# Kernel tuning notes

Measured on AMD Instinct MI355X. Metric: run time of the kernel, lower is better.

## Reference

```python
import jax, jax.numpy as jnp
import numpy as np

H = 64          # hiddens_dims
K = 3           # Chebyshev order
B = 16          # graphs in batch
NPG = 16384     # nodes per graph
N = B * NPG     # total nodes
E = 2_097_152   # total edges
R = 2191        # num_residues (hard-coded in source)
E_REF = R * 16
HALF = N // 2   # backbone count == sidechain count (mask is balanced per graph)


def _lin(k, fan_in, shape):
    return jax.random.uniform(k, shape, jnp.float32, -1.0, 1.0) / np.sqrt(fan_in)


def setup_inputs() -> dict:
    key = jax.random.key(0)
    ks = jax.random.split(key, 40)
    inp = {}
    inp["x"] = jax.random.normal(ks[0], (N, 3), jnp.float32)
    inp["edge_index"] = jax.random.randint(ks[1], (2, E), 0, N)
    inp["batch"] = jnp.repeat(jnp.arange(B, dtype=jnp.int32), NPG)
    blk = jnp.concatenate([jnp.ones((NPG // 2,), bool), jnp.zeros((NPG // 2,), bool)])
    inp["mask"] = jnp.tile(blk, B)  # backbone=True first half of each graph block
    inp["x_ref"] = jax.random.normal(ks[2], (R, 3), jnp.float32)
    inp["edgeref"] = jax.random.randint(ks[3], (2, E_REF), 0, R)
    i = 4
    for name, cin in [("cw0", 3), ("cw1", H), ("cw2", H), ("rw0", 3), ("rw1", H), ("rw2", H)]:
        inp[name] = _lin(ks[i], cin, (K, cin, H)); i += 1
        inp[name.replace("w", "b")] = jnp.zeros((H,), jnp.float32)  # ChebConv bias init = zeros
    for name, cin, cout in [("mlp_w", 2 * H, H), ("mlpP2_w", 2 * H, H),
                            ("rep0_w", H, H), ("rep1_w", H, H), ("rep2_w", H, 3)]:
        inp[name] = _lin(ks[i], cin, (cin, cout)); i += 1
        inp[name.replace("_w", "_b")] = _lin(ks[i], cin, (cout,)); i += 1
    return inp


def cheb_conv(x, edge_index, W, b, n):
    # PyG ChebConv with sym normalization, lambda_max=2: L_hat = -D^-1/2 A D^-1/2 (diag = 0)
    row, col = edge_index[0], edge_index[1]
    deg = jax.ops.segment_sum(jnp.ones_like(x[:, 0])[row] * 0 + 1.0, row, num_segments=n)
    dinv = jnp.where(deg > 0, jax.lax.rsqrt(jnp.maximum(deg, 1e-12)), 0.0)
    w = -(dinv[row] * dinv[col])  # [E]

    def prop(h):  # L_hat @ h via gather + segment_sum
        return jax.ops.segment_sum(w[:, None] * h[col], row, num_segments=n)

    Tx0 = x
    out = Tx0 @ W[0]
    Tx1 = prop(x)
    out = out + Tx1 @ W[1]
    for k in range(2, K):
        Tx2 = 2.0 * prop(Tx1) - Tx0
        out = out + Tx2 @ W[k]
        Tx0, Tx1 = Tx1, Tx2
    return out + b


def _forward(x, edge_index, mask, x_ref, edgeref,
             cw0, cb0, cw1, cb1, cw2, cb2, rw0, rb0, rw1, rb1, rw2, rb2,
             mlp_w, mlp_b, mlpP2_w, mlpP2_b,
             rep0_w, rep0_b, rep1_w, rep1_b, rep2_w, rep2_b):
    # main GNN stack (tanh after all but last; dropout is identity in eval)
    h = jnp.tanh(cheb_conv(x, edge_index, cw0, cb0, N))
    h = jnp.tanh(cheb_conv(h, edge_index, cw1, cb1, N))
    h = cheb_conv(h, edge_index, cw2, cb2, N)

    bb_idx = jnp.nonzero(mask, size=HALF)[0]
    sc_idx = jnp.nonzero(~mask, size=HALF)[0]
    x_bb = h[bb_idx].reshape(B, -1, H).mean(axis=1)[:, None, :]  # [B,1,H]
    x_sc = h[sc_idx].reshape(B, -1, H).mean(axis=1)[:, None, :]  # [B,1,H]

    # reference-graph stack: source bug makes `conv2 != self.convs[-1]` always True,
    # so tanh follows every convRef layer
    r = jnp.tanh(cheb_conv(x_ref, edgeref, rw0, rb0, R))
    r = jnp.tanh(cheb_conv(r, edgeref, rw1, rb1, R))
    r = jnp.tanh(cheb_conv(r, edgeref, rw2, rb2, R))
    r = jnp.broadcast_to(r[None], (B, R, H))

    bb_rep = jnp.broadcast_to(x_bb, (B, R, H))
    phase1 = jnp.concatenate([r, bb_rep], axis=-1) @ mlp_w + mlp_b        # [B,R,H]
    sc_rep = jnp.broadcast_to(x_sc, (B, R, H))
    phase2 = jnp.concatenate([phase1, sc_rep], axis=-1) @ mlpP2_w + mlpP2_b  # [B,R,H]

    res = phase2.reshape(-1, H)
    res = jax.nn.relu(res @ rep0_w + rep0_b)
    res = jax.nn.relu(res @ rep1_w + rep1_b)
    res = jax.nn.relu(res @ rep2_w + rep2_b)  # [B*R, 3]
    return res.reshape(-1, 3), x_bb, x_sc


def reference(x, edge_index, batch, mask, x_ref, edgeref,
              cw0, cb0, cw1, cb1, cw2, cb2, rw0, rb0, rw1, rb1, rw2, rb2,
              mlp_w, mlp_b, mlpP2_w, mlpP2_b,
              rep0_w, rep0_b, rep1_w, rep1_b, rep2_w, rep2_b):
    del batch  # only used for len(batch.unique()) == B, a static constant here
    return _forward(x, edge_index, mask, x_ref, edgeref,
                    cw0, cb0, cw1, cb1, cw2, cb2, rw0, rb0, rw1, rb1, rw2, rb2,
                    mlp_w, mlp_b, mlpP2_w, mlpP2_b,
                    rep0_w, rep0_b, rep1_w, rep1_b, rep2_w, rep2_b)
```

## Files before the change

kernel.cpp:

```cpp
#include <hip/hip_runtime.h>
#include <hip/hip_fp16.h>
#include <math.h>

#define NN 262144
#define NE 2097152
#define RR 2191
#define ER (RR*16)
#define NB 16
#define BRR (NB*RR)
#define OUT_RES (BRR*3)

typedef __attribute__((ext_vector_type(8))) _Float16 half8;
typedef __attribute__((ext_vector_type(4))) float f32x4;

__global__ void k_hist(const int* __restrict__ row, int* __restrict__ deg, int nE){
  int i = blockIdx.x*blockDim.x + threadIdx.x;
  int st = gridDim.x*blockDim.x;
  for (; i < nE; i += st) atomicAdd(&deg[row[i]], 1);
}

__global__ void k_dinv(const int* __restrict__ deg, float* __restrict__ dinv, int n){
  int i = blockIdx.x*blockDim.x + threadIdx.x;
  if (i < n){ int d = deg[i]; dinv[i] = d > 0 ? 1.0f/sqrtf((float)d) : 0.0f; }
}

__global__ void k_scan1(const int* __restrict__ deg, int* __restrict__ rowptr, int* __restrict__ partials){
  __shared__ int s[256];
  int t = threadIdx.x; int i = blockIdx.x*256 + t;
  int v = deg[i]; s[t] = v; __syncthreads();
  for (int off = 1; off < 256; off <<= 1){
    int x = (t >= off) ? s[t-off] : 0; __syncthreads();
    s[t] += x; __syncthreads();
  }
  rowptr[i] = s[t] - v;
  if (t == 255) partials[blockIdx.x] = s[255];
}

__global__ void k_scan2(int* __restrict__ partials){
  __shared__ int s[1024];
  int t = threadIdx.x; int v = partials[t]; s[t] = v; __syncthreads();
  for (int off = 1; off < 1024; off <<= 1){
    int x = (t >= off) ? s[t-off] : 0; __syncthreads();
    s[t] += x; __syncthreads();
  }
  partials[t] = s[t] - v;
}

__global__ void k_scan3(int* __restrict__ rowptr, const int* __restrict__ partials){
  int t = threadIdx.x; int i = blockIdx.x*256 + t;
  rowptr[i] += partials[blockIdx.x];
  if (i == 0) rowptr[NN] = NE;
}

__global__ void k_scan_small(const int* __restrict__ deg, int* __restrict__ rowptr, int n){
  __shared__ int s[256];
  int t = threadIdx.x;
  int carry = 0;
  for (int base = 0; base < n; base += 256){
    int idx = base + t;
    int v = (idx < n) ? deg[idx] : 0;
    s[t] = v; __syncthreads();
    for (int off = 1; off < 256; off <<= 1){
      int x = (t >= off) ? s[t-off] : 0; __syncthreads();
      s[t] += x; __syncthreads();
    }
    if (idx < n) rowptr[idx] = carry + s[t] - v;
    carry += s[255];
    __syncthreads();
  }
  if (t == 0) rowptr[n] = carry;
}

__global__ void k_scatter(const int* __restrict__ row, const int* __restrict__ col,
                          const float* __restrict__ dinv, const int* __restrict__ rowptr,
                          int* __restrict__ cursor, int2* __restrict__ pair, int nE){
  int i = blockIdx.x*blockDim.x + threadIdx.x;
  int st = gridDim.x*blockDim.x;
  for (; i < nE; i += st){
    int r = row[i], c = col[i];
    int pos = rowptr[r] + atomicAdd(&cursor[r], 1);
    pair[pos] = make_int2(c, __float_as_int(-dinv[r]*dinv[c]));
  }
}

__global__ void k_prop3(const float* __restrict__ h, float* __restrict__ y,
                        const int* __restrict__ rowptr, const int2* __restrict__ pair, int n){
  int i = blockIdx.x*blockDim.x + threadIdx.x;
  if (i >= n) return;
  float a0 = 0.f, a1 = 0.f, a2 = 0.f;
  int s = rowptr[i], e = rowptr[i+1];
  int p = s;
  for (; p + 4 <= e; p += 4){
    int2 q0 = pair[p], q1 = pair[p+1], q2 = pair[p+2], q3 = pair[p+3];
    float w0 = __int_as_float(q0.y), w1 = __int_as_float(q1.y);
    float w2 = __int_as_float(q2.y), w3 = __int_as_float(q3.y);
    float x00=h[q0.x*3+0], x01=h[q0.x*3+1], x02=h[q0.x*3+2];
    float x10=h[q1.x*3+0], x11=h[q1.x*3+1], x12=h[q1.x*3+2];
    float x20=h[q2.x*3+0], x21=h[q2.x*3+1], x22=h[q2.x*3+2];
    float x30=h[q3.x*3+0], x31=h[q3.x*3+1], x32=h[q3.x*3+2];
    a0 = fmaf(w0,x00, fmaf(w1,x10, fmaf(w2,x20, fmaf(w3,x30, a0))));
    a1 = fmaf(w0,x01, fmaf(w1,x11, fmaf(w2,x21, fmaf(w3,x31, a1))));
    a2 = fmaf(w0,x02, fmaf(w1,x12, fmaf(w2,x22, fmaf(w3,x32, a2))));
  }
  for (; p < e; p++){
    int2 q = pair[p]; float wv = __int_as_float(q.y);
    a0 = fmaf(wv, h[q.x*3+0], a0); a1 = fmaf(wv, h[q.x*3+1], a1); a2 = fmaf(wv, h[q.x*3+2], a2);
  }
  y[i*3+0] = a0; y[i*3+1] = a1; y[i*3+2] = a2;
}

__global__ void k_prop64(const float* __restrict__ h, float* __restrict__ y,
                         const int* __restrict__ rowptr, const int2* __restrict__ pair, int n){
  int t = threadIdx.x, lane = t & 63;
  int i = blockIdx.x*4 + (t >> 6);
  if (i >= n) return;
  float acc = 0.f;
  int s = rowptr[i], e = rowptr[i+1];
  int p = s;
  for (; p + 4 <= e; p += 4){
    int2 q0 = pair[p], q1 = pair[p+1], q2 = pair[p+2], q3 = pair[p+3];
    float v0 = h[(size_t)q0.x*64 + lane], v1 = h[(size_t)q1.x*64 + lane];
    float v2 = h[(size_t)q2.x*64 + lane], v3 = h[(size_t)q3.x*64 + lane];
    acc = fmaf(__int_as_float(q0.y),v0, fmaf(__int_as_float(q1.y),v1,
          fmaf(__int_as_float(q2.y),v2, fmaf(__int_as_float(q3.y),v3, acc))));
  }
  for (; p < e; p++){
    int2 q = pair[p];
    acc = fmaf(__int_as_float(q.y), h[(size_t)q.x*64 + lane], acc);
  }
  y[(size_t)i*64 + lane] = acc;
}

__global__ void __launch_bounds__(256) k_prop64h(
    const uint2* __restrict__ h2, uint2* __restrict__ y2,
    const int* __restrict__ rowptr, const int2* __restrict__ pair, int n){
  int t = threadIdx.x;
  int sub = t & 15;
  int row = blockIdx.x*16 + (t >> 4);
  if (row >= n) return;
  int s = rowptr[row], e = rowptr[row+1];
  float a0=0.f, a1=0.f, a2=0.f, a3=0.f;
  int p = s;
  for (; p + 4 <= e; p += 4){
    int2 q0 = pair[p], q1 = pair[p+1], q2 = pair[p+2], q3 = pair[p+3];
    uint2 v0 = h2[(size_t)q0.x*16 + sub];
    uint2 v1 = h2[(size_t)q1.x*16 + sub];
    uint2 v2 = h2[(size_t)q2.x*16 + sub];
    uint2 v3 = h2[(size_t)q3.x*16 + sub];
    float w0 = __int_as_float(q0.y), w1 = __int_as_float(q1.y);
    float w2 = __int_as_float(q2.y), w3 = __int_as_float(q3.y);
    float2 f0a = __half22float2(*(__half2*)&v0.x), f0b = __half22float2(*(__half2*)&v0.y);
    float2 f1a = __half22float2(*(__half2*)&v1.x), f1b = __half22float2(*(__half2*)&v1.y);
    float2 f2a = __half22float2(*(__half2*)&v2.x), f2b = __half22float2(*(__half2*)&v2.y);
    float2 f3a = __half22float2(*(__half2*)&v3.x), f3b = __half22float2(*(__half2*)&v3.y);
    a0 = fmaf(w0,f0a.x, fmaf(w1,f1a.x, fmaf(w2,f2a.x, fmaf(w3,f3a.x, a0))));
    a1 = fmaf(w0,f0a.y, fmaf(w1,f1a.y, fmaf(w2,f2a.y, fmaf(w3,f3a.y, a1))));
    a2 = fmaf(w0,f0b.x, fmaf(w1,f1b.x, fmaf(w2,f2b.x, fmaf(w3,f3b.x, a2))));
    a3 = fmaf(w0,f0b.y, fmaf(w1,f1b.y, fmaf(w2,f2b.y, fmaf(w3,f3b.y, a3))));
  }
  for (; p < e; p++){
    int2 q = pair[p];
    float wv = __int_as_float(q.y);
    uint2 v = h2[(size_t)q.x*16 + sub];
    float2 fa = __half22float2(*(__half2*)&v.x), fb = __half22float2(*(__half2*)&v.y);
    a0 = fmaf(wv, fa.x, a0); a1 = fmaf(wv, fa.y, a1);
    a2 = fmaf(wv, fb.x, a2); a3 = fmaf(wv, fb.y, a3);
  }
  __half2 lo = __floats2half2_rn(a0, a1), hi = __floats2half2_rn(a2, a3);
  uint2 r; r.x = *(unsigned*)&lo; r.y = *(unsigned*)&hi;
  y2[(size_t)row*16 + sub] = r;
}

__global__ void k_combine3f(const float* __restrict__ x, const float* __restrict__ t1,
                            const float* __restrict__ t2, const float* __restrict__ W,
                            const float* __restrict__ bias, float* __restrict__ out, int n){
  int t = threadIdx.x, lane = t & 63;
  int i = blockIdx.x*4 + (t >> 6);
  if (i >= n) return;
  float acc = bias[lane];
  #pragma unroll
  for (int j = 0; j < 3; j++){
    float x0 = x[i*3+j], x1 = t1[i*3+j];
    float x2 = 2.0f*t2[i*3+j] - x0;
    acc += x0*W[      j*64 + lane]
         + x1*W[192 + j*64 + lane]
         + x2*W[384 + j*64 + lane];
  }
  out[(size_t)i*64 + lane] = tanhf(acc);
}

__global__ void k_combine3h(const float* __restrict__ x, const float* __restrict__ t1,
                            const float* __restrict__ t2, const float* __restrict__ W,
                            const float* __restrict__ bias, __half* __restrict__ out, int n){
  int t = threadIdx.x, lane = t & 63;
  int i = blockIdx.x*4 + (t >> 6);
  if (i >= n) return;
  float acc = bias[lane];
  #pragma unroll
  for (int j = 0; j < 3; j++){
    float x0 = x[i*3+j], x1 = t1[i*3+j];
    float x2 = 2.0f*t2[i*3+j] - x0;
    acc += x0*W[      j*64 + lane]
         + x1*W[192 + j*64 + lane]
         + x2*W[384 + j*64 + lane];
  }
  out[(size_t)i*64 + lane] = __float2half_rn(tanhf(acc));
}

__global__ void k_weff(const float* __restrict__ W, float* __restrict__ D){
  int i = blockIdx.x*blockDim.x + threadIdx.x;
  D[i]        = W[i] - W[8192 + i];
  D[4096 + i] = W[4096 + i];
  D[8192 + i] = 2.0f * W[8192 + i];
}

__global__ void k_wpack(const float* __restrict__ W, _Float16* __restrict__ D){
  int t = blockIdx.x*blockDim.x + threadIdx.x;
  int reg = t & 7, lane = (t >> 3) & 63, nt = (t >> 9) & 3, kc = t >> 11;
  int m = kc >> 1;
  int kin = (kc & 1)*32 + ((lane >> 4) & 3)*8 + reg;
  int n = nt*16 + (lane & 15);
  float eff;
  if      (m == 0) eff = W[kin*64 + n] - W[8192 + kin*64 + n];
  else if (m == 1) eff = W[4096 + kin*64 + n];
  else             eff = 2.0f * W[8192 + kin*64 + n];
  D[t] = (_Float16)eff;
}

__global__ void __launch_bounds__(256) k_combine64m(
    const __half* A, const __half* B, const __half* C,
    const _Float16* __restrict__ wfrag, const float* __restrict__ bias,
    __half* out, int ntiles, int wavestride){
  int t = threadIdx.x;
  int lane = t & 63;
  int wv = blockIdx.x*4 + (t >> 6);
  half8 bf[24];
  #pragma unroll
  for (int i = 0; i < 24; i++)
    bf[i] = *(const half8*)(wfrag + ((size_t)(i*64 + lane))*8);
  int col = lane & 15, grp = (lane >> 4) & 3;
  float b0 = bias[col], b1 = bias[16+col], b2 = bias[32+col], b3 = bias[48+col];
  for (int tile = wv; tile < ntiles; tile += wavestride){
    size_t rb = (size_t)tile*16;
    f32x4 acc0 = {b0,b0,b0,b0}, acc1 = {b1,b1,b1,b1};
    f32x4 acc2 = {b2,b2,b2,b2}, acc3 = {b3,b3,b3,b3};
    #pragma unroll
    for (int kc = 0; kc < 6; kc++){
      const __half* s = (kc < 2) ? A : (kc < 4) ? B : C;
      half8 a = *(const half8*)(s + (rb + col)*64 + (kc & 1)*32 + grp*8);
      acc0 = __builtin_amdgcn_mfma_f32_16x16x32_f16(a, bf[kc*4+0], acc0, 0,0,0);
      acc1 = __builtin_amdgcn_mfma_f32_16x16x32_f16(a, bf[kc*4+1], acc1, 0,0,0);
      acc2 = __builtin_amdgcn_mfma_f32_16x16x32_f16(a, bf[kc*4+2], acc2, 0,0,0);
      acc3 = __builtin_amdgcn_mfma_f32_16x16x32_f16(a, bf[kc*4+3], acc3, 0,0,0);
    }
    __half* o = out + (rb + grp*4)*64;
    #pragma unroll
    for (int r = 0; r < 4; r++){
      o[(size_t)r*64 +      col] = __float2half_rn(tanhf(acc0[r]));
      o[(size_t)r*64 + 16 + col] = __float2half_rn(tanhf(acc1[r]));
      o[(size_t)r*64 + 32 + col] = __float2half_rn(tanhf(acc2[r]));
      o[(size_t)r*64 + 48 + col] = __float2half_rn(tanhf(acc3[r]));
    }
  }
}

__global__ void k_pool3(const __half2* __restrict__ hA, const __half2* __restrict__ hB,
                        const __half2* __restrict__ hC, float* __restrict__ pA,
                        float* __restrict__ pB, float* __restrict__ pC){
  const __half2* src = (blockIdx.y == 0) ? hA : (blockIdx.y == 1) ? hB : hC;
  float* dst         = (blockIdx.y == 0) ? pA : (blockIdx.y == 1) ? pB : pC;
  int blk = blockIdx.x;
  int chunk = blk & 15, seg = blk >> 4;
  int t = threadIdx.x, ch2 = t & 31, rsub = t >> 5;
  int base = seg*8192 + chunk*512;
  float ax = 0.f, ay = 0.f;
  for (int j = 0; j < 64; j++){
    int row = base + rsub + j*8;
    float2 v = __half22float2(src[(size_t)row*32 + ch2]);
    ax += v.x; ay += v.y;
  }
  __shared__ float sx[256], sy[256];
  sx[t] = ax; sy[t] = ay; __syncthreads();
  if (t < 32){
    float tx = 0.f, ty = 0.f;
    #pragma unroll
    for (int j = 0; j < 8; j++){ tx += sx[ch2 + j*32]; ty += sy[ch2 + j*32]; }
    int b = seg >> 1, half_ = seg & 1;
    atomicAdd(&dst[half_*1024 + b*64 + ch2*2],     tx);
    atomicAdd(&dst[half_*1024 + b*64 + ch2*2 + 1], ty);
  }
}

__global__ void k_combine_pooled(const float* __restrict__ pA, const float* __restrict__ pB,
                                 const float* __restrict__ pC, const float* __restrict__ weff,
                                 const float* __restrict__ bias, float* __restrict__ xbbsc,
                                 float* __restrict__ dout){
  int i = blockIdx.x*blockDim.x + threadIdx.x;
  int pr = i >> 6, c = i & 63;
  const float* a = pA + pr*64;
  const float* b = pB + pr*64;
  const float* cc = pC + pr*64;
  float v = 0.f;
  for (int k = 0; k < 64; k++){
    v = fmaf(a[k],  weff[        k*64 + c], v);
    v = fmaf(b[k],  weff[4096 +  k*64 + c], v);
    v = fmaf(cc[k], weff[8192 +  k*64 + c], v);
  }
  v = v*(1.0f/8192.0f) + bias[c];
  xbbsc[i] = v;
  dout[OUT_RES + i] = v;
}

__global__ void __launch_bounds__(256) k_combine64f(
    const float* __restrict__ A, const float* __restrict__ Bm, const float* __restrict__ C,
    const float* __restrict__ Weff, const float* __restrict__ bias,
    float* __restrict__ out, int n){
  int t = threadIdx.x;
  int lane = t & 63;
  int wid  = __builtin_amdgcn_readfirstlane(t >> 6);
  int half_ = wid & 1;
  int row  = blockIdx.x*128 + (wid >> 1)*64 + lane;
  bool active = (row < n);
  float acc[32];
  #pragma unroll
  for (int c = 0; c < 32; c++) acc[c] = bias[half_*32 + c];
  if (active){
    #pragma unroll 1
    for (int m = 0; m < 3; m++){
      const float* src = (m == 0 ? A : (m == 1 ? Bm : C)) + (size_t)row*64;
      const float* Wm  = Weff + m*4096 + half_*32;
      #pragma unroll 1
      for (int k4 = 0; k4 < 16; k4++){
        float4 a4 = *(const float4*)(src + k4*4);
        const float* wk = Wm + k4*256;
        #pragma unroll
        for (int kk = 0; kk < 4; kk++){
          float a = (kk == 0) ? a4.x : (kk == 1) ? a4.y : (kk == 2) ? a4.z : a4.w;
          #pragma unroll
          for (int c = 0; c < 32; c++)
            acc[c] = fmaf(a, wk[kk*64 + c], acc[c]);
        }
      }
    }
  }
  __syncthreads();
  if (active){
    float* o = out + (size_t)row*64 + half_*32;
    #pragma unroll
    for (int c = 0; c < 32; c++) o[c] = tanhf(acc[c]);
  }
}

__global__ void k_matrows(const float* __restrict__ in, const float* __restrict__ W,
                          const float* __restrict__ bias, float* __restrict__ out,
                          int n, int accum){
  int t = threadIdx.x, lane = t & 63;
  int i = blockIdx.x*4 + (t >> 6);
  if (i >= n) return;
  float v = in[i*64 + lane];
  float acc = bias ? bias[lane] : 0.0f;
  #pragma unroll
  for (int k = 0; k < 64; k++) acc += __shfl(v, k, 64) * W[k*64 + lane];
  if (accum) acc += out[i*64 + lane];
  out[i*64 + lane] = acc;
}

__global__ void k_final(const float* __restrict__ rt3, const float* __restrict__ bt3,
                        const float* __restrict__ W1, const float* __restrict__ b1,
                        const float* __restrict__ W2, const float* __restrict__ b2,
                        float* __restrict__ dout){
  int t = threadIdx.x, lane = t & 63;
  int g = blockIdx.x*4 + (t >> 6);
  if (g >= BRR) return;
  int b = g / RR, r = g - b*RR;
  float m = rt3[r*64 + lane] + bt3[b*64 + lane];
  m = fmaxf(m, 0.0f);
  float acc = b1[lane];
  #pragma unroll
  for (int k = 0; k < 64; k++) acc += __shfl(m, k, 64) * W1[k*64 + lane];
  float u = fmaxf(acc, 0.0f);
  float p0 = u*W2[lane*3+0], p1 = u*W2[lane*3+1], p2 = u*W2[lane*3+2];
  #pragma unroll
  for (int off = 32; off > 0; off >>= 1){
    p0 += __shfl_xor(p0, off, 64);
    p1 += __shfl_xor(p1, off, 64);
    p2 += __shfl_xor(p2, off, 64);
  }
  if (lane == 0){
    dout[g*3+0] = fmaxf(p0 + b2[0], 0.0f);
    dout[g*3+1] = fmaxf(p1 + b2[1], 0.0f);
    dout[g*3+2] = fmaxf(p2 + b2[2], 0.0f);
  }
}

extern "C" void kernel_launch(void* const* d_in, const int* in_sizes, int n_in,
                              void* d_out, int out_size, void* d_ws, size_t ws_size,
                              hipStream_t stream){
  const float* x     = (const float*)d_in[0];
  const int*   eidx  = (const int*)d_in[1];
  const float* x_ref = (const float*)d_in[4];
  const int*   eref  = (const int*)d_in[5];
  const float* cw0 = (const float*)d_in[6],  *cb0 = (const float*)d_in[7];
  const float* cw1 = (const float*)d_in[8],  *cb1 = (const float*)d_in[9];
  const float* cw2 = (const float*)d_in[10], *cb2 = (const float*)d_in[11];
  const float* rw0 = (const float*)d_in[12], *rb0 = (const float*)d_in[13];
  const float* rw1 = (const float*)d_in[14], *rb1 = (const float*)d_in[15];
  const float* rw2 = (const float*)d_in[16], *rb2 = (const float*)d_in[17];
  const float* mlp_w  = (const float*)d_in[18], *mlp_b  = (const float*)d_in[19];
  const float* mlp2_w = (const float*)d_in[20], *mlp2_b = (const float*)d_in[21];
  const float* rep0_w = (const float*)d_in[22], *rep0_b = (const float*)d_in[23];
  const float* rep1_w = (const float*)d_in[24], *rep1_b = (const float*)d_in[25];
  const float* rep2_w = (const float*)d_in[26], *rep2_b = (const float*)d_in[27];
  float* out = (float*)d_out;

  char* w = (char*)d_ws;
  size_t off = 0;
  auto alloc = [&](size_t bytes)->void*{
    void* p = w + off;
    off = (off + bytes + 255) & ~(size_t)255;
    return p;
  };
  int*   deg     = (int*)  alloc(NN*4);
  int*   cursor  = (int*)  alloc(NN*4);
  int*   degR    = (int*)  alloc(RR*4);
  int*   cursorR = (int*)  alloc(RR*4);
  float* poolA   = (float*)alloc(2048*4);
  float* poolB   = (float*)alloc(2048*4);
  float* poolC   = (float*)alloc(2048*4);
  size_t zero_bytes = off;

  int*   rowptr   = (int*)  alloc((NN+1)*4);
  int*   partials = (int*)  alloc(1024*4);
  int*   rowptrR  = (int*)  alloc((RR+1)*4);
  float* dinv     = (float*)alloc(NN*4);
  float* dinvR    = (float*)alloc(RR*4);
  int2*  cpair    = (int2*) alloc((size_t)NE*8);
  int2*  cpairR   = (int2*) alloc((size_t)ER*8);
  float* t1_3     = (float*)alloc((size_t)NN*3*4);
  float* t2_3     = (float*)alloc((size_t)NN*3*4);
  float* rt1_3    = (float*)alloc(RR*3*4);
  float* rt2_3    = (float*)alloc(RR*3*4);
  __half* hA      = (__half*)alloc((size_t)NN*64*2);
  __half* hB      = (__half*)alloc((size_t)NN*64*2);
  __half* hC      = (__half*)alloc((size_t)NN*64*2);
  float* refA     = (float*)alloc(RR*64*4);
  float* refB     = (float*)alloc(RR*64*4);
  float* refC     = (float*)alloc(RR*64*4);
  float* xbbsc    = (float*)alloc(2048*4);
  float* rterm    = (float*)alloc(RR*64*4);
  float* bbterm   = (float*)alloc(NB*64*4);
  float* rt2a     = (float*)alloc(RR*64*4);
  float* bt2a     = (float*)alloc(NB*64*4);
  float* rt3a     = (float*)alloc(RR*64*4);
  float* bt3a     = (float*)alloc(NB*64*4);
  float* weffC2   = (float*)alloc(12288*4);
  float* weffR1   = (float*)alloc(12288*4);
  float* weffR2   = (float*)alloc(12288*4);
  _Float16* wfragC1 = (_Float16*)alloc(12288*2);
  (void)ws_size; (void)in_sizes; (void)n_in; (void)out_size;

  hipMemsetAsync(d_ws, 0, zero_bytes, stream);

  k_weff<<<16, 256, 0, stream>>>(cw2, weffC2);
  k_weff<<<16, 256, 0, stream>>>(rw1, weffR1);
  k_weff<<<16, 256, 0, stream>>>(rw2, weffR2);
  k_wpack<<<48, 256, 0, stream>>>(cw1, wfragC1);

  k_hist<<<2048, 256, 0, stream>>>(eidx, deg, NE);
  k_hist<<<64,   256, 0, stream>>>(eref, degR, ER);
  k_dinv<<<1024, 256, 0, stream>>>(deg, dinv, NN);
  k_dinv<<<9,    256, 0, stream>>>(degR, dinvR, RR);
  k_scan1<<<1024, 256, 0, stream>>>(deg, rowptr, partials);
  k_scan2<<<1, 1024, 0, stream>>>(partials);
  k_scan3<<<1024, 256, 0, stream>>>(rowptr, partials);
  k_scan_small<<<1, 256, 0, stream>>>(degR, rowptrR, RR);
  k_scatter<<<2048, 256, 0, stream>>>(eidx, eidx+NE, dinv, rowptr, cursor, cpair, NE);
  k_scatter<<<64,   256, 0, stream>>>(eref, eref+ER, dinvR, rowptrR, cursorR, cpairR, ER);

  k_prop3<<<1024, 256, 0, stream>>>(x, t1_3, rowptr, cpair, NN);
  k_prop3<<<1024, 256, 0, stream>>>(t1_3, t2_3, rowptr, cpair, NN);
  k_combine3h<<<NN/4, 256, 0, stream>>>(x, t1_3, t2_3, cw0, cb0, hA, NN);
  k_prop64h<<<NN/16, 256, 0, stream>>>((const uint2*)hA, (uint2*)hB, rowptr, cpair, NN);
  k_prop64h<<<NN/16, 256, 0, stream>>>((const uint2*)hB, (uint2*)hC, rowptr, cpair, NN);
  k_combine64m<<<1024, 256, 0, stream>>>(hA, hB, hC, wfragC1, cb1, hA, NN/16, 4096);
  k_prop64h<<<NN/16, 256, 0, stream>>>((const uint2*)hA, (uint2*)hB, rowptr, cpair, NN);
  k_prop64h<<<NN/16, 256, 0, stream>>>((const uint2*)hB, (uint2*)hC, rowptr, cpair, NN);
  k_pool3<<<dim3(512,3), 256, 0, stream>>>((const __half2*)hA, (const __half2*)hB,
                                           (const __half2*)hC, poolA, poolB, poolC);
  k_combine_pooled<<<8, 256, 0, stream>>>(poolA, poolB, poolC, weffC2, cb2, xbbsc, out);

  k_prop3<<<9, 256, 0, stream>>>(x_ref, rt1_3, rowptrR, cpairR, RR);
  k_prop3<<<9, 256, 0, stream>>>(rt1_3, rt2_3, rowptrR, cpairR, RR);
  k_combine3f<<<548, 256, 0, stream>>>(x_ref, rt1_3, rt2_3, rw0, rb0, refA, RR);
  k_prop64<<<548, 256, 0, stream>>>(refA, refB, rowptrR, cpairR, RR);
  k_prop64<<<548, 256, 0, stream>>>(refB, refC, rowptrR, cpairR, RR);
  k_combine64f<<<(RR+127)/128, 256, 0, stream>>>(refA, refB, refC, weffR1, rb1, refA, RR);
  k_prop64<<<548, 256, 0, stream>>>(refA, refB, rowptrR, cpairR, RR);
  k_prop64<<<548, 256, 0, stream>>>(refB, refC, rowptrR, cpairR, RR);
  k_combine64f<<<(RR+127)/128, 256, 0, stream>>>(refA, refB, refC, weffR2, rb2, refA, RR);

  k_matrows<<<548, 256, 0, stream>>>(refA,   mlp_w,        nullptr, rterm,  RR, 0);
  k_matrows<<<4,   256, 0, stream>>>(xbbsc,  mlp_w+4096,   mlp_b,   bbterm, NB, 0);
  k_matrows<<<548, 256, 0, stream>>>(rterm,  mlp2_w,       nullptr, rt2a,   RR, 0);
  k_matrows<<<4,   256, 0, stream>>>(bbterm, mlp2_w,       nullptr, bt2a,   NB, 0);
  k_matrows<<<4,   256, 0, stream>>>(xbbsc+1024, mlp2_w+4096, mlp2_b, bt2a, NB, 1);
  k_matrows<<<548, 256, 0, stream>>>(rt2a,   rep0_w,       nullptr, rt3a,   RR, 0);
  k_matrows<<<4,   256, 0, stream>>>(bt2a,   rep0_w,       rep0_b,  bt3a,   NB, 0);

  k_final<<<(BRR+3)/4, 256, 0, stream>>>(rt3a, bt3a, rep1_w, rep1_b, rep2_w, rep2_b, out);
}
```

Baseline: 760.1 us.

## Two-pass bucketed CSR build, fuse dinv into scans, fuse MLP chains, wider gather unroll

Replaces the per-row atomic scatter for the CSR build with a two-pass scheme. Edges are first binned into 64-row buckets through a small atomic counter array, then a per-bucket kernel places them into rows using shared-memory cursors. This is meant to cut contention on global atomics and scattered writes, at the cost of an extra staging buffer and an extra pass over the edges. The dinv computation is folded into the scan kernels, the seven small matrix-row launches become two chained kernels, and the fp16 propagation gather is unrolled to 8 edges for more memory-level parallelism.

```diff
diff --git a/kernel.cpp b/kernel.cpp
--- a/kernel.cpp
+++ b/kernel.cpp
@@ -9,6 +9,7 @@
 #define NB 16
 #define BRR (NB*RR)
 #define OUT_RES (BRR*3)
+#define NBKT 4096
 
 typedef __attribute__((ext_vector_type(8))) _Float16 half8;
 typedef __attribute__((ext_vector_type(4))) float f32x4;
@@ -19,15 +20,12 @@
   for (; i < nE; i += st) atomicAdd(&deg[row[i]], 1);
 }
 
-__global__ void k_dinv(const int* __restrict__ deg, float* __restrict__ dinv, int n){
-  int i = blockIdx.x*blockDim.x + threadIdx.x;
-  if (i < n){ int d = deg[i]; dinv[i] = d > 0 ? 1.0f/sqrtf((float)d) : 0.0f; }
-}
-
-__global__ void k_scan1(const int* __restrict__ deg, int* __restrict__ rowptr, int* __restrict__ partials){
+__global__ void k_scan1(const int* __restrict__ deg, int* __restrict__ rowptr,
+                        int* __restrict__ partials, float* __restrict__ dinv){
   __shared__ int s[256];
   int t = threadIdx.x; int i = blockIdx.x*256 + t;
   int v = deg[i]; s[t] = v; __syncthreads();
+  dinv[i] = v > 0 ? 1.0f/sqrtf((float)v) : 0.0f;
   for (int off = 1; off < 256; off <<= 1){
     int x = (t >= off) ? s[t-off] : 0; __syncthreads();
     s[t] += x; __syncthreads();
@@ -52,13 +50,15 @@
   if (i == 0) rowptr[NN] = NE;
 }
 
-__global__ void k_scan_small(const int* __restrict__ deg, int* __restrict__ rowptr, int n){
+__global__ void k_scan_small(const int* __restrict__ deg, int* __restrict__ rowptr,
+                             float* __restrict__ dinv, int n){
   __shared__ int s[256];
   int t = threadIdx.x;
   int carry = 0;
   for (int base = 0; base < n; base += 256){
     int idx = base + t;
     int v = (idx < n) ? deg[idx] : 0;
+    if (idx < n) dinv[idx] = v > 0 ? 1.0f/sqrtf((float)v) : 0.0f;
     s[t] = v; __syncthreads();
     for (int off = 1; off < 256; off <<= 1){
       int x = (t >= off) ? s[t-off] : 0; __syncthreads();
@@ -71,9 +71,44 @@
   if (t == 0) rowptr[n] = carry;
 }
 
-__global__ void k_scatter(const int* __restrict__ row, const int* __restrict__ col,
-                          const float* __restrict__ dinv, const int* __restrict__ rowptr,
-                          int* __restrict__ cursor, int2* __restrict__ pair, int nE){
+__global__ void k_binA(const int* __restrict__ row, const int* __restrict__ col,
+                       const float* __restrict__ dinv, const int* __restrict__ rowptr,
+                       int* __restrict__ bcur, int2* __restrict__ staging, int nE){
+  int i = blockIdx.x*blockDim.x + threadIdx.x;
+  int st = gridDim.x*blockDim.x;
+  for (; i < nE; i += st){
+    int r = row[i], c = col[i];
+    int b = r >> 6;
+    int pos = rowptr[b << 6] + atomicAdd(&bcur[b], 1);
+    float wv = -dinv[r]*dinv[c];
+    staging[pos] = make_int2(((r & 63) << 24) | c, __float_as_int(wv));
+  }
+}
+
+__global__ void __launch_bounds__(256) k_binB(const int2* __restrict__ staging,
+                                              const int* __restrict__ rowptr,
+                                              int2* __restrict__ cpair){
+  __shared__ int rp[65];
+  __shared__ int rowcur[64];
+  int b = blockIdx.x;
+  int t = threadIdx.x;
+  if (t < 64){ rowcur[t] = 0; rp[t] = rowptr[(b << 6) + t]; }
+  if (t == 64) rp[64] = rowptr[(b << 6) + 64];
+  __syncthreads();
+  int base = rp[0];
+  int n_b = rp[64] - base;
+  for (int i = t; i < n_b; i += 256){
+    int2 pr = staging[base + i];
+    int rl = (pr.x >> 24) & 63;
+    int c  = pr.x & 0xFFFFFF;
+    int idx = atomicAdd(&rowcur[rl], 1);
+    cpair[rp[rl] + idx] = make_int2(c, pr.y);
+  }
+}
+
+__global__ void k_scatter_ref(const int* __restrict__ row, const int* __restrict__ col,
+                              const float* __restrict__ dinv, const int* __restrict__ rowptr,
+                              int* __restrict__ cursor, int2* __restrict__ pair, int nE){
   int i = blockIdx.x*blockDim.x + threadIdx.x;
   int st = gridDim.x*blockDim.x;
   for (; i < nE; i += st){
@@ -141,22 +176,35 @@
   int s = rowptr[row], e = rowptr[row+1];
   float a0=0.f, a1=0.f, a2=0.f, a3=0.f;
   int p = s;
+  for (; p + 8 <= e; p += 8){
+    int2 q[8]; uint2 v[8];
+    #pragma unroll
+    for (int j = 0; j < 8; j++) q[j] = pair[p+j];
+    #pragma unroll
+    for (int j = 0; j < 8; j++) v[j] = h2[(size_t)q[j].x*16 + sub];
+    #pragma unroll
+    for (int j = 0; j < 8; j++){
+      float wv = __int_as_float(q[j].y);
+      float2 fa = __half22float2(*(__half2*)&v[j].x);
+      float2 fb = __half22float2(*(__half2*)&v[j].y);
+      a0 = fmaf(wv, fa.x, a0); a1 = fmaf(wv, fa.y, a1);
+      a2 = fmaf(wv, fb.x, a2); a3 = fmaf(wv, fb.y, a3);
+    }
+  }
   for (; p + 4 <= e; p += 4){
-    int2 q0 = pair[p], q1 = pair[p+1], q2 = pair[p+2], q3 = pair[p+3];
-    uint2 v0 = h2[(size_t)q0.x*16 + sub];
-    uint2 v1 = h2[(size_t)q1.x*16 + sub];
-    uint2 v2 = h2[(size_t)q2.x*16 + sub];
-    uint2 v3 = h2[(size_t)q3.x*16 + sub];
-    float w0 = __int_as_float(q0.y), w1 = __int_as_float(q1.y);
-    float w2 = __int_as_float(q2.y), w3 = __int_as_float(q3.y);
-    float2 f0a = __half22float2(*(__half2*)&v0.x), f0b = __half22float2(*(__half2*)&v0.y);
-    float2 f1a = __half22float2(*(__half2*)&v1.x), f1b = __half22float2(*(__half2*)&v1.y);
-    float2 f2a = __half22float2(*(__half2*)&v2.x), f2b = __half22float2(*(__half2*)&v2.y);
-    float2 f3a = __half22float2(*(__half2*)&v3.x), f3b = __half22float2(*(__half2*)&v3.y);
-    a0 = fmaf(w0,f0a.x, fmaf(w1,f1a.x, fmaf(w2,f2a.x, fmaf(w3,f3a.x, a0))));
-    a1 = fmaf(w0,f0a.y, fmaf(w1,f1a.y, fmaf(w2,f2a.y, fmaf(w3,f3a.y, a1))));
-    a2 = fmaf(w0,f0b.x, fmaf(w1,f1b.x, fmaf(w2,f2b.x, fmaf(w3,f3b.x, a2))));
-    a3 = fmaf(w0,f0b.y, fmaf(w1,f1b.y, fmaf(w2,f2b.y, fmaf(w3,f3b.y, a3))));
+    int2 q[4]; uint2 v[4];
+    #pragma unroll
+    for (int j = 0; j < 4; j++) q[j] = pair[p+j];
+    #pragma unroll
+    for (int j = 0; j < 4; j++) v[j] = h2[(size_t)q[j].x*16 + sub];
+    #pragma unroll
+    for (int j = 0; j < 4; j++){
+      float wv = __int_as_float(q[j].y);
+      float2 fa = __half22float2(*(__half2*)&v[j].x);
+      float2 fb = __half22float2(*(__half2*)&v[j].y);
+      a0 = fmaf(wv, fa.x, a0); a1 = fmaf(wv, fa.y, a1);
+      a2 = fmaf(wv, fb.x, a2); a3 = fmaf(wv, fb.y, a3);
+    }
   }
   for (; p < e; p++){
     int2 q = pair[p];
@@ -351,18 +399,47 @@
   }
 }
 
-__global__ void k_matrows(const float* __restrict__ in, const float* __restrict__ W,
-                          const float* __restrict__ bias, float* __restrict__ out,
-                          int n, int accum){
+__global__ void k_refchain(const float* __restrict__ refA, const float* __restrict__ mlp_w,
+                           const float* __restrict__ mlp2_w, const float* __restrict__ rep0_w,
+                           float* __restrict__ rt3a, int n){
   int t = threadIdx.x, lane = t & 63;
   int i = blockIdx.x*4 + (t >> 6);
   if (i >= n) return;
-  float v = in[i*64 + lane];
-  float acc = bias ? bias[lane] : 0.0f;
-  #pragma unroll
-  for (int k = 0; k < 64; k++) acc += __shfl(v, k, 64) * W[k*64 + lane];
-  if (accum) acc += out[i*64 + lane];
-  out[i*64 + lane] = acc;
+  float v = refA[i*64 + lane];
+  float a = 0.f;
+  #pragma unroll
+  for (int k = 0; k < 64; k++) a += __shfl(v, k, 64) * mlp_w[k*64 + lane];
+  float b = 0.f;
+  #pragma unroll
+  for (int k = 0; k < 64; k++) b += __shfl(a, k, 64) * mlp2_w[k*64 + lane];
+  float c = 0.f;
+  #pragma unroll
+  for (int k = 0; k < 64; k++) c += __shfl(b, k, 64) * rep0_w[k*64 + lane];
+  rt3a[i*64 + lane] = c;
+}
+
+__global__ void k_bbchain(const float* __restrict__ xbbsc,
+                          const float* __restrict__ mlp_w,  const float* __restrict__ mlp_b,
+                          const float* __restrict__ mlp2_w, const float* __restrict__ mlp2_b,
+                          const float* __restrict__ rep0_w, const float* __restrict__ rep0_b,
+                          float* __restrict__ bt3a){
+  int t = threadIdx.x, lane = t & 63;
+  int i = blockIdx.x*4 + (t >> 6);
+  if (i >= NB) return;
+  float vbb = xbbsc[i*64 + lane];
+  float vsc = xbbsc[1024 + i*64 + lane];
+  float a = mlp_b[lane];
+  #pragma unroll
+  for (int k = 0; k < 64; k++) a += __shfl(vbb, k, 64) * mlp_w[4096 + k*64 + lane];
+  float b = mlp2_b[lane];
+  #pragma unroll
+  for (int k = 0; k < 64; k++) b += __shfl(a, k, 64) * mlp2_w[k*64 + lane];
+  #pragma unroll
+  for (int k = 0; k < 64; k++) b += __shfl(vsc, k, 64) * mlp2_w[4096 + k*64 + lane];
+  float c = rep0_b[lane];
+  #pragma unroll
+  for (int k = 0; k < 64; k++) c += __shfl(b, k, 64) * rep0_w[k*64 + lane];
+  bt3a[i*64 + lane] = c;
 }
 
 __global__ void k_final(const float* __restrict__ rt3, const float* __restrict__ bt3,
@@ -421,7 +498,7 @@
     return p;
   };
   int*   deg     = (int*)  alloc(NN*4);
-  int*   cursor  = (int*)  alloc(NN*4);
+  int*   bcur    = (int*)  alloc(NBKT*4);
   int*   degR    = (int*)  alloc(RR*4);
   int*   cursorR = (int*)  alloc(RR*4);
   float* poolA   = (float*)alloc(2048*4);
@@ -434,6 +511,7 @@
   int*   rowptrR  = (int*)  alloc((RR+1)*4);
   float* dinv     = (float*)alloc(NN*4);
   float* dinvR    = (float*)alloc(RR*4);
+  int2*  staging  = (int2*) alloc((size_t)NE*8);
   int2*  cpair    = (int2*) alloc((size_t)NE*8);
   int2*  cpairR   = (int2*) alloc((size_t)ER*8);
   float* t1_3     = (float*)alloc((size_t)NN*3*4);
@@ -447,10 +525,6 @@
   float* refB     = (float*)alloc(RR*64*4);
   float* refC     = (float*)alloc(RR*64*4);
   float* xbbsc    = (float*)alloc(2048*4);
-  float* rterm    = (float*)alloc(RR*64*4);
-  float* bbterm   = (float*)alloc(NB*64*4);
-  float* rt2a     = (float*)alloc(RR*64*4);
-  float* bt2a     = (float*)alloc(NB*64*4);
   float* rt3a     = (float*)alloc(RR*64*4);
   float* bt3a     = (float*)alloc(NB*64*4);
   float* weffC2   = (float*)alloc(12288*4);
@@ -468,14 +542,13 @@
 
   k_hist<<<2048, 256, 0, stream>>>(eidx, deg, NE);
   k_hist<<<64,   256, 0, stream>>>(eref, degR, ER);
-  k_dinv<<<1024, 256, 0, stream>>>(deg, dinv, NN);
-  k_dinv<<<9,    256, 0, stream>>>(degR, dinvR, RR);
-  k_scan1<<<1024, 256, 0, stream>>>(deg, rowptr, partials);
+  k_scan1<<<1024, 256, 0, stream>>>(deg, rowptr, partials, dinv);
   k_scan2<<<1, 1024, 0, stream>>>(partials);
   k_scan3<<<1024, 256, 0, stream>>>(rowptr, partials);
-  k_scan_small<<<1, 256, 0, stream>>>(degR, rowptrR, RR);
-  k_scatter<<<2048, 256, 0, stream>>>(eidx, eidx+NE, dinv, rowptr, cursor, cpair, NE);
-  k_scatter<<<64,   256, 0, stream>>>(eref, eref+ER, dinvR, rowptrR, cursorR, cpairR, ER);
+  k_scan_small<<<1, 256, 0, stream>>>(degR, rowptrR, dinvR, RR);
+  k_binA<<<2048, 256, 0, stream>>>(eidx, eidx+NE, dinv, rowptr, bcur, staging, NE);
+  k_binB<<<NBKT, 256, 0, stream>>>(staging, rowptr, cpair);
+  k_scatter_ref<<<64, 256, 0, stream>>>(eref, eref+ER, dinvR, rowptrR, cursorR, cpairR, ER);
 
   k_prop3<<<1024, 256, 0, stream>>>(x, t1_3, rowptr, cpair, NN);
   k_prop3<<<1024, 256, 0, stream>>>(t1_3, t2_3, rowptr, cpair, NN);
@@ -499,13 +572,8 @@
   k_prop64<<<548, 256, 0, stream>>>(refB, refC, rowptrR, cpairR, RR);
   k_combine64f<<<(RR+127)/128, 256, 0, stream>>>(refA, refB, refC, weffR2, rb2, refA, RR);
 
-  k_matrows<<<548, 256, 0, stream>>>(refA,   mlp_w,        nullptr, rterm,  RR, 0);
-  k_matrows<<<4,   256, 0, stream>>>(xbbsc,  mlp_w+4096,   mlp_b,   bbterm, NB, 0);
-  k_matrows<<<548, 256, 0, stream>>>(rterm,  mlp2_w,       nullptr, rt2a,   RR, 0);
-  k_matrows<<<4,   256, 0, stream>>>(bbterm, mlp2_w,       nullptr, bt2a,   NB, 0);
-  k_matrows<<<4,   256, 0, stream>>>(xbbsc+1024, mlp2_w+4096, mlp2_b, bt2a, NB, 1);
-  k_matrows<<<548, 256, 0, stream>>>(rt2a,   rep0_w,       nullptr, rt3a,   RR, 0);
-  k_matrows<<<4,   256, 0, stream>>>(bt2a,   rep0_w,       rep0_b,  bt3a,   NB, 0);
+  k_refchain<<<548, 256, 0, stream>>>(refA, mlp_w, mlp2_w, rep0_w, rt3a, RR);
+  k_bbchain<<<4, 256, 0, stream>>>(xbbsc, mlp_w, mlp_b, mlp2_w, mlp2_b, rep0_w, rep0_b, bt3a);
 
   k_final<<<(BRR+3)/4, 256, 0, stream>>>(rt3a, bt3a, rep1_w, rep1_b, rep2_w, rep2_b, out);
 }
```

Result: slower. 839.9 us (+10.5%).
